# Kernel tuning notes

Measured on AMD Instinct MI355X. Metric: run time of the kernel, lower is better.

## Reference

```python
import jax, jax.numpy as jnp
import numpy as np

LATENT_N = 1024
COMMITMENT_COST = 1.0
TEMP = 0.1


def setup_inputs() -> dict:
    key = jax.random.key(0)
    k0, k1, k2, k3, k4, k5 = jax.random.split(key, 6)
    N, D, H, Fd, K = 65536, 1024, 128, 512, LATENT_N
    input_data = jax.random.normal(k0, (N, D), dtype=jnp.float32)
    W1 = jax.random.normal(k1, (D, H), dtype=jnp.float32) * (1.0 / np.sqrt(D))
    b1 = jnp.zeros((H,), dtype=jnp.float32)
    W2 = jax.random.normal(k2, (H, Fd), dtype=jnp.float32) * (1.0 / np.sqrt(H))
    b2 = jnp.zeros((Fd,), dtype=jnp.float32)
    code_book = jax.random.uniform(k3, (K, Fd), dtype=jnp.float32,
                                   minval=-1.0 / K, maxval=1.0 / K)
    return {"input_data": input_data, "W1": W1, "b1": b1,
            "W2": W2, "b2": b2, "code_book": code_book}


def reference(input_data, W1, b1, W2, b2, code_book):
    # feat MLP: Linear -> ReLU -> Linear
    z = jnp.matmul(jnp.maximum(jnp.matmul(input_data, W1) + b1, 0.0), W2) + b2  # [N, F]
    # squared L2 distances to codebook entries: [N, K]
    distances = (jnp.sum(z * z, axis=1, keepdims=True)
                 + jnp.sum(code_book * code_book, axis=1)
                 - 2.0 * jnp.matmul(z, code_book.T))
    logits = -distances / TEMP
    # categorical sample per row (softmax of logits)
    idx = jax.random.categorical(jax.random.key(42), logits, axis=-1)  # [N] int
    encodings = jax.nn.one_hot(idx, LATENT_N, dtype=z.dtype)  # [N, K]
    quantized = jnp.matmul(encodings, code_book)  # [N, F] == code_book[idx]
    e_latent_loss = jnp.mean((jax.lax.stop_gradient(quantized) - z) ** 2)
    q_latent_loss = jnp.mean((quantized - jax.lax.stop_gradient(z)) ** 2)
    loss = q_latent_loss + COMMITMENT_COST * e_latent_loss
    # straight-through estimator
    quantized_st = z + jax.lax.stop_gradient(quantized - z)
    avg_probs = jnp.mean(encodings, axis=0)  # [K]
    perplexity = jnp.exp(-jnp.sum(avg_probs * jnp.log(avg_probs + 1e-10)))
    return (loss, quantized_st, perplexity, encodings, -distances)
```

## Files before the change

kernel.cpp:

```cpp
#include <hip/hip_runtime.h>
#include <stdint.h>

#define N_ROWS 65536
#define DIM 1024
#define HID 128
#define FD 512
#define KCB 1024
#define HALFCNT 33554432u

#define OFF_Q    1
#define OFF_PERP 33554433
#define OFF_ENC  33554434
#define OFF_ND   100663298

typedef __attribute__((ext_vector_type(8))) short sh8;
typedef __attribute__((ext_vector_type(4))) float f32x4;

__device__ __forceinline__ uint32_t rotl32(uint32_t v, int r) { return (v << r) | (v >> (32 - r)); }

__device__ __forceinline__ void threefry(uint32_t c0, uint32_t c1, uint32_t& o0, uint32_t& o1) {
    const uint32_t ks0 = 0u, ks1 = 42u, ks2 = 0x1BD11BDAu ^ 0u ^ 42u;
    uint32_t x0 = c0 + ks0, x1 = c1 + ks1;
#define TFR(r) x0 += x1; x1 = rotl32(x1, r); x1 ^= x0;
    TFR(13) TFR(15) TFR(26) TFR(6)  x0 += ks1; x1 += ks2 + 1u;
    TFR(17) TFR(29) TFR(16) TFR(24) x0 += ks2; x1 += ks0 + 2u;
    TFR(13) TFR(15) TFR(26) TFR(6)  x0 += ks0; x1 += ks1 + 3u;
    TFR(17) TFR(29) TFR(16) TFR(24) x0 += ks1; x1 += ks2 + 4u;
    TFR(13) TFR(15) TFR(26) TFR(6)  x0 += ks2; x1 += ks0 + 5u;
#undef TFR
    o0 = x0; o1 = x1;
}

__device__ __forceinline__ float gumbel_f32(uint32_t b) {
    uint32_t m = b >> 9;
    float u = m ? (float)m * 1.1920928955078125e-07f : 1.17549435e-38f;
    const float LN2 = 0.6931471805599453f;
    return -LN2 * __log2f(-LN2 * __log2f(u));
}

__device__ __forceinline__ ushort bf16rne(float f) {
    uint32_t u = __float_as_uint(f);
    return (ushort)((u + 0x7FFFu + ((u >> 16) & 1u)) >> 16);
}
__device__ __forceinline__ uint32_t pack2rne(float a, float b) {
    return (uint32_t)bf16rne(a) | ((uint32_t)bf16rne(b) << 16);
}

__device__ __forceinline__ void async_cp16(const void* g, void* l) {
    __builtin_amdgcn_global_load_lds(
        (const __attribute__((address_space(1))) void*)g,
        (__attribute__((address_space(3))) void*)l, 16, 0, 0);
}

__global__ __launch_bounds__(256) void k_prep(const float* __restrict__ cb, const float* __restrict__ W1,
                                              const float* __restrict__ W2,
                                              ushort* __restrict__ cbh, double* __restrict__ cc,
                                              ushort* __restrict__ w1th, ushort* __restrict__ w2th,
                                              int* __restrict__ counts, double* __restrict__ lossb) {
    int gb = blockIdx.x, t = threadIdx.x;
    if (gb < 256) {
        int k = gb * 4 + (t >> 6), l = t & 63;
        const float4* row = (const float4*)(cb + (size_t)k * FD);
        float4 a = row[l * 2], b = row[l * 2 + 1];
        float v[8] = {a.x, a.y, a.z, a.w, b.x, b.y, b.z, b.w};
        double s = 0.0;
        uint32_t hu[4];
        #pragma unroll
        for (int e = 0; e < 4; ++e) {
            hu[e] = pack2rne(v[2 * e], v[2 * e + 1]);
            s = fma((double)v[2 * e], (double)v[2 * e], s);
            s = fma((double)v[2 * e + 1], (double)v[2 * e + 1], s);
        }
        *(uint4*)(cbh + (size_t)k * FD + l * 8) = make_uint4(hu[0], hu[1], hu[2], hu[3]);
        for (int off = 32; off; off >>= 1) s += __shfl_down(s, off, 64);
        if (l == 0) cc[k] = s;
    } else if (gb < 384) {
        int c = gb - 256;
        #pragma unroll
        for (int u = 0; u < 4; ++u) {
            int k = t + u * 256;
            w1th[(size_t)c * DIM + k] = bf16rne(W1[(size_t)k * HID + c]);
        }
    } else if (gb < 640) {
        int c = (gb - 384) * 2 + (t >> 7);
        int tt = t & 127;
        w2th[(size_t)c * HID + tt] = bf16rne(W2[(size_t)tt * FD + c]);
    } else {
        for (int k = t; k < KCB; k += 256) counts[k] = 0;
        lossb[t] = 0.0;
    }
}

__global__ __launch_bounds__(256) void kAB(const float* __restrict__ X, const ushort* __restrict__ w1th,
                                           const float* __restrict__ b1, const ushort* __restrict__ w2th,
                                           const float* __restrict__ b2,
                                           ushort* __restrict__ zbh, float* __restrict__ zz) {
    __shared__ __align__(16) char lds[32768];
    __shared__ float zzp[128][2];
    int t = threadIdx.x;
    int lane = t & 63, w = t >> 6;
    int wr = w >> 1, wc = w & 1;
    int lane15 = lane & 15, lg = lane >> 4;
    int n0 = blockIdx.x * 128;
    f32x4 zero4 = {0.f, 0.f, 0.f, 0.f};
    f32x4 acc[4][4];
    #pragma unroll
    for (int i = 0; i < 4; ++i)
        #pragma unroll
        for (int j = 0; j < 4; ++j) acc[i][j] = zero4;

    int xr = t >> 1;
    int cb0 = (t & 1) * 4;
    int xsw = xr & 7;

    for (int k0 = 0; k0 < DIM; k0 += 64) {
        #pragma unroll
        for (int i = 0; i < 4; ++i) {
            int rr = w * 32 + i * 8;
            int row = rr + (lane >> 3);
            int csrc = (lane & 7) ^ (row & 7);
            size_t goff = (size_t)row * DIM + k0 + csrc * 8;
            async_cp16(w1th + goff, lds + 16384 + rr * 128);
        }
        const float* xp = X + (size_t)(n0 + xr) * DIM + k0 + cb0 * 8;
        #pragma unroll
        for (int c = 0; c < 4; ++c) {
            float4 a = *(const float4*)(xp + c * 8);
            float4 b = *(const float4*)(xp + c * 8 + 4);
            uint4 hv;
            hv.x = pack2rne(a.x, a.y);
            hv.y = pack2rne(a.z, a.w);
            hv.z = pack2rne(b.x, b.y);
            hv.w = pack2rne(b.z, b.w);
            int slot = xr * 128 + (((cb0 + c) ^ xsw) << 4);
            *(uint4*)(lds + slot) = hv;
        }
        __syncthreads();
        #pragma unroll
        for (int kh = 0; kh < 2; ++kh) {
            int ch = kh * 4 + lg;
            sh8 ah[4], bh[4];
            #pragma unroll
            for (int i = 0; i < 4; ++i) {
                int ra = wr * 64 + i * 16 + lane15;
                ah[i] = *(const sh8*)(lds + ra * 128 + ((ch ^ (ra & 7)) << 4));
            }
            #pragma unroll
            for (int j = 0; j < 4; ++j) {
                int rb = wc * 64 + j * 16 + lane15;
                bh[j] = *(const sh8*)(lds + 16384 + rb * 128 + ((ch ^ (rb & 7)) << 4));
            }
            #pragma unroll
            for (int i = 0; i < 4; ++i)
                #pragma unroll
                for (int j = 0; j < 4; ++j)
                    acc[i][j] = __builtin_amdgcn_mfma_f32_16x16x32_bf16(ah[i], bh[j], acc[i][j], 0, 0, 0);
        }
        __syncthreads();
    }
    #pragma unroll
    for (int j = 0; j < 4; ++j) {
        int hcol = wc * 64 + j * 16 + lane15;
        float b1v = b1[hcol];
        int k8 = hcol >> 3, klo = hcol & 7;
        #pragma unroll
        for (int i = 0; i < 4; ++i)
            #pragma unroll
            for (int r = 0; r < 4; ++r) {
                int row = wr * 64 + i * 16 + lg * 4 + r;
                ushort hb = bf16rne(fmaxf(acc[i][j][r] + b1v, 0.f));
                *(ushort*)(lds + row * 256 + ((k8 ^ (row & 7)) << 4) + klo * 2) = hb;
            }
    }
    __syncthreads();
    float zsum[16];
    #pragma unroll
    for (int e = 0; e < 16; ++e) zsum[e] = 0.f;
    for (int c2 = 0; c2 < 4; ++c2) {
        f32x4 acc2[4][4];
        #pragma unroll
        for (int i = 0; i < 4; ++i)
            #pragma unroll
            for (int j = 0; j < 4; ++j) acc2[i][j] = zero4;
        #pragma unroll
        for (int kh = 0; kh < 4; ++kh) {
            int ch = kh * 4 + lg;
            sh8 ah[4], bh[4];
            #pragma unroll
            for (int i = 0; i < 4; ++i) {
                int ra = wr * 64 + i * 16 + lane15;
                ah[i] = *(const sh8*)(lds + ra * 256 + ((ch ^ (ra & 7)) << 4));
            }
            #pragma unroll
            for (int j = 0; j < 4; ++j) {
                int col = c2 * 128 + wc * 64 + j * 16 + lane15;
                bh[j] = *(const sh8*)(w2th + (size_t)col * HID + ch * 8);
            }
            #pragma unroll
            for (int i = 0; i < 4; ++i)
                #pragma unroll
                for (int j = 0; j < 4; ++j)
                    acc2[i][j] = __builtin_amdgcn_mfma_f32_16x16x32_bf16(ah[i], bh[j], acc2[i][j], 0, 0, 0);
        }
        #pragma unroll
        for (int j = 0; j < 4; ++j) {
            int col = c2 * 128 + wc * 64 + j * 16 + lane15;
            float b2v = b2[col];
            #pragma unroll
            for (int i = 0; i < 4; ++i)
                #pragma unroll
                for (int r = 0; r < 4; ++r) {
                    int row = wr * 64 + i * 16 + lg * 4 + r;
                    float v = acc2[i][j][r] + b2v;
                    zbh[(size_t)(n0 + row) * FD + col] = bf16rne(v);
                    zsum[i * 4 + r] = fmaf(v, v, zsum[i * 4 + r]);
                }
        }
    }
    #pragma unroll
    for (int e = 0; e < 16; ++e) {
        float s = zsum[e];
        s += __shfl_xor(s, 1, 64); s += __shfl_xor(s, 2, 64);
        s += __shfl_xor(s, 4, 64); s += __shfl_xor(s, 8, 64);
        if (lane15 == 0) zzp[wr * 64 + (e >> 2) * 16 + lg * 4 + (e & 3)][wc] = s;
    }
    __syncthreads();
    if (t < 128) zz[n0 + t] = zzp[t][0] + zzp[t][1];
}

__global__ __launch_bounds__(256) void k_mfma3s(const ushort* __restrict__ zbh, const ushort* __restrict__ cbh,
                                                const float* __restrict__ zz, const double* __restrict__ cc,
                                                float* __restrict__ nd,
                                                unsigned long long* __restrict__ partials) {
    __shared__ __align__(16) char lds[32768];
    int t = threadIdx.x;
    int lane = t & 63, w = t >> 6;
    int wr = w >> 1, wc = w & 1;
    int bid = blockIdx.x;
    int bm = ((bid >> 6) << 3) | (bid & 7);
    int bkn = (bid >> 3) & 7;
    const ushort* Ahg = zbh + (size_t)bm * 128 * FD;
    const ushort* Bhg = cbh + (size_t)bkn * 128 * FD;

    f32x4 zero4 = {0.f, 0.f, 0.f, 0.f};
    f32x4 acc[4][4];
    #pragma unroll
    for (int i = 0; i < 4; ++i)
        #pragma unroll
        for (int j = 0; j < 4; ++j) acc[i][j] = zero4;

    for (int k0 = 0; k0 < FD; k0 += 64) {
        #pragma unroll
        for (int i = 0; i < 4; ++i) {
            int rr = w * 32 + i * 8;
            int row = rr + (lane >> 3);
            int csrc = (lane & 7) ^ (row & 7);
            size_t goff = (size_t)row * FD + k0 + csrc * 8;
            async_cp16(Ahg + goff, lds + rr * 128);
            async_cp16(Bhg + goff, lds + 16384 + rr * 128);
        }
        __syncthreads();
        #pragma unroll
        for (int kh = 0; kh < 2; ++kh) {
            int ch = kh * 4 + (lane >> 4);
            sh8 ah[4], bh[4];
            #pragma unroll
            for (int i = 0; i < 4; ++i) {
                int ra = wr * 64 + i * 16 + (lane & 15);
                ah[i] = *(const sh8*)(lds + ra * 128 + ((ch ^ (ra & 7)) << 4));
            }
            #pragma unroll
            for (int j = 0; j < 4; ++j) {
                int rb = wc * 64 + j * 16 + (lane & 15);
                bh[j] = *(const sh8*)(lds + 16384 + rb * 128 + ((ch ^ (rb & 7)) << 4));
            }
            #pragma unroll
            for (int i = 0; i < 4; ++i)
                #pragma unroll
                for (int j = 0; j < 4; ++j)
                    acc[i][j] = __builtin_amdgcn_mfma_f32_16x16x32_bf16(ah[i], bh[j], acc[i][j], 0, 0, 0);
        }
        __syncthreads();
    }
    int lane15 = lane & 15, lg = lane >> 4;
    int gcol[4];
    double ccv[4];
    #pragma unroll
    for (int j = 0; j < 4; ++j) {
        gcol[j] = bkn * 128 + wc * 64 + j * 16 + lane15;
        ccv[j] = cc[gcol[j]];
    }
    bool high = bm >= 256;
    uint32_t csub = high ? HALFCNT : 0u;
    #pragma unroll
    for (int i = 0; i < 4; ++i)
        #pragma unroll
        for (int r = 0; r < 4; ++r) {
            int grow = bm * 128 + wr * 64 + i * 16 + lg * 4 + r;
            float zzf = zz[grow];
            double zv = (double)zzf;
            size_t rowoff = (size_t)grow << 10;
            unsigned long long bkey = 0ull;
            #pragma unroll
            for (int j = 0; j < 4; ++j) {
                float ndf = (float)(2.0 * (double)acc[i][j][r] - zv - ccv[j]);
                nd[rowoff + gcol[j]] = ndf;
                uint32_t iflat = (uint32_t)grow * 1024u + (uint32_t)gcol[j];
                uint32_t base = iflat - csub;
                uint32_t r0, r1;
                threefry(base, base + HALFCNT, r0, r1);
                float gv = gumbel_f32(high ? r1 : r0);
                float s = (ndf + zzf) * 10.0f + gv;
                uint32_t ub = __float_as_uint(s);
                ub ^= (uint32_t)(((int32_t)ub >> 31) | 0x80000000);
                unsigned long long key = ((unsigned long long)ub << 32) | (uint32_t)(1023 - gcol[j]);
                if (key > bkey) bkey = key;
            }
            #pragma unroll
            for (int m = 1; m <= 8; m <<= 1) {
                unsigned long long o = __shfl_xor(bkey, m, 64);
                if (o > bkey) bkey = o;
            }
            if (lane15 == 0) partials[(size_t)grow * 16 + bkn * 2 + wc] = bkey;
        }
}

__global__ __launch_bounds__(256) void k_enc2(const unsigned long long* __restrict__ partials,
                                              const float* __restrict__ nd, const float* __restrict__ cb,
                                              float* __restrict__ enc, float* __restrict__ qz,
                                              int* __restrict__ counts, double* __restrict__ lossb) {
    int t = threadIdx.x;
    int n0 = blockIdx.x * 16;
    __shared__ int si[16];
    if (t < 16) {
        int n = n0 + t;
        const unsigned long long* p = partials + (size_t)n * 16;
        unsigned long long best = p[0];
        #pragma unroll
        for (int e = 1; e < 16; ++e) {
            unsigned long long v = p[e];
            if (v > best) best = v;
        }
        int k = 1023 - (int)(best & 0xFFFFFFFFull);
        si[t] = k;
        atomicAdd(&counts[k], 1);
        float ndv = nd[(size_t)n * KCB + k];
        atomicAdd(&lossb[n & 255], -(double)ndv);
    }
    __syncthreads();
    #pragma unroll
    for (int r = 0; r < 16; ++r) {
        int id = si[r];
        int base = t * 4;
        float4 v;
        v.x = (id == base)     ? 1.0f : 0.0f;
        v.y = (id == base + 1) ? 1.0f : 0.0f;
        v.z = (id == base + 2) ? 1.0f : 0.0f;
        v.w = (id == base + 3) ? 1.0f : 0.0f;
        *(float4*)&enc[(size_t)(n0 + r) * KCB + base] = v;
    }
    for (int e = t; e < 16 * 128; e += 256) {
        int r = e >> 7, s = e & 127;
        *(float4*)&qz[(size_t)(n0 + r) * FD + s * 4] =
            *(const float4*)&cb[(size_t)si[r] * FD + s * 4];
    }
}

__global__ void k_scalars(const int* __restrict__ counts, const double* __restrict__ lossb,
                          float* __restrict__ out) {
    int t = threadIdx.x;
    double s = 0.0;
    for (int k = t; k < KCB; k += 256) {
        double p = (double)counts[k] * (1.0 / 65536.0);
        s += p * log(p + 1e-10);
    }
    double lsum = lossb[t];
    for (int off = 32; off; off >>= 1) {
        s += __shfl_down(s, off, 64);
        lsum += __shfl_down(lsum, off, 64);
    }
    __shared__ double red[4], redl[4];
    int lane = t & 63, w = t >> 6;
    if (lane == 0) { red[w] = s; redl[w] = lsum; }
    __syncthreads();
    if (t == 0) {
        double tot = red[0] + red[1] + red[2] + red[3];
        double ltot = redl[0] + redl[1] + redl[2] + redl[3];
        out[OFF_PERP] = (float)exp(-tot);
        out[0] = (float)(ltot * (2.0 / 33554432.0));
    }
}

extern "C" void kernel_launch(void* const* d_in, const int* in_sizes, int n_in,
                              void* d_out, int out_size, void* d_ws, size_t ws_size,
                              hipStream_t stream) {
    const float* X  = (const float*)d_in[0];
    const float* W1 = (const float*)d_in[1];
    const float* b1 = (const float*)d_in[2];
    const float* W2 = (const float*)d_in[3];
    const float* b2 = (const float*)d_in[4];
    const float* cb = (const float*)d_in[5];

    float* out = (float*)d_out;
    float* qz  = out + (size_t)OFF_Q;
    float* enc = out + (size_t)OFF_ENC;
    float* nd  = out + (size_t)OFF_ND;

    float* zz = (float*)d_ws;
    double* cc = (double*)(zz + 65536);
    double* lossb = cc + 1024;
    int* counts = (int*)(lossb + 256);

    bool big_ws = ws_size >= ((size_t)100 << 20);
    char* big = big_ws ? ((char*)d_ws + (1 << 20)) : (char*)(enc + 2);
    unsigned long long* partials = (unsigned long long*)big;
    ushort* ub   = (ushort*)(big + ((size_t)9 << 20));
    ushort* zbh  = ub;
    ushort* cbh  = ub + 33554432;
    ushort* w1th = ub + 34078720;
    ushort* w2th = ub + 34209792;

    k_prep<<<641, 256, 0, stream>>>(cb, W1, W2, cbh, cc, w1th, w2th, counts, lossb);
    kAB<<<512, 256, 0, stream>>>(X, w1th, b1, w2th, b2, zbh, zz);
    k_mfma3s<<<4096, 256, 0, stream>>>(zbh, cbh, zz, cc, nd, partials);
    k_enc2<<<4096, 256, 0, stream>>>(partials, nd, cb, enc, qz, counts, lossb);
    k_scalars<<<1, 256, 0, stream>>>(counts, lossb, out);
}
```

Baseline: 472.1 us.

## Fuse distance GEMM, Gumbel argmax and encoding into one row-block kernel

The distance GEMM, Gumbel-max sampling, partial-argmax merge, one-hot and quantized writes are merged into one kernel. Each block owns 64 rows and loops over all 1024 codebook entries, keeping the z tile in LDS and reading codebook fragments straight from global memory. This drops the partials buffer round trip, the reread of nd for the loss, and one kernel launch. The MLP kernel's row tile is also halved to 64 to launch more blocks. The trade-offs are 64KB of LDS per block, lower occupancy, and codebook operands read from global instead of staged tiles.

```diff
diff --git a/kernel.cpp b/kernel.cpp
--- a/kernel.cpp
+++ b/kernel.cpp
@@ -95,22 +95,22 @@
                                            const float* __restrict__ b1, const ushort* __restrict__ w2th,
                                            const float* __restrict__ b2,
                                            ushort* __restrict__ zbh, float* __restrict__ zz) {
-    __shared__ __align__(16) char lds[32768];
-    __shared__ float zzp[128][2];
+    __shared__ __align__(16) char lds[24576];
+    __shared__ float zzp[64][2];
     int t = threadIdx.x;
     int lane = t & 63, w = t >> 6;
     int wr = w >> 1, wc = w & 1;
     int lane15 = lane & 15, lg = lane >> 4;
-    int n0 = blockIdx.x * 128;
+    int n0 = blockIdx.x * 64;
     f32x4 zero4 = {0.f, 0.f, 0.f, 0.f};
-    f32x4 acc[4][4];
-    #pragma unroll
-    for (int i = 0; i < 4; ++i)
+    f32x4 acc[2][4];
+    #pragma unroll
+    for (int i = 0; i < 2; ++i)
         #pragma unroll
         for (int j = 0; j < 4; ++j) acc[i][j] = zero4;
 
-    int xr = t >> 1;
-    int cb0 = (t & 1) * 4;
+    int xr = t >> 2;
+    int cq = (t & 3) * 2;
     int xsw = xr & 7;
 
     for (int k0 = 0; k0 < DIM; k0 += 64) {
@@ -119,12 +119,11 @@
             int rr = w * 32 + i * 8;
             int row = rr + (lane >> 3);
             int csrc = (lane & 7) ^ (row & 7);
-            size_t goff = (size_t)row * DIM + k0 + csrc * 8;
-            async_cp16(w1th + goff, lds + 16384 + rr * 128);
-        }
-        const float* xp = X + (size_t)(n0 + xr) * DIM + k0 + cb0 * 8;
-        #pragma unroll
-        for (int c = 0; c < 4; ++c) {
+            async_cp16(w1th + (size_t)row * DIM + k0 + csrc * 8, lds + 8192 + rr * 128);
+        }
+        const float* xp = X + (size_t)(n0 + xr) * DIM + k0 + cq * 8;
+        #pragma unroll
+        for (int c = 0; c < 2; ++c) {
             float4 a = *(const float4*)(xp + c * 8);
             float4 b = *(const float4*)(xp + c * 8 + 4);
             uint4 hv;
@@ -132,26 +131,25 @@
             hv.y = pack2rne(a.z, a.w);
             hv.z = pack2rne(b.x, b.y);
             hv.w = pack2rne(b.z, b.w);
-            int slot = xr * 128 + (((cb0 + c) ^ xsw) << 4);
-            *(uint4*)(lds + slot) = hv;
+            *(uint4*)(lds + xr * 128 + (((cq + c) ^ xsw) << 4)) = hv;
         }
         __syncthreads();
         #pragma unroll
         for (int kh = 0; kh < 2; ++kh) {
             int ch = kh * 4 + lg;
-            sh8 ah[4], bh[4];
-            #pragma unroll
-            for (int i = 0; i < 4; ++i) {
-                int ra = wr * 64 + i * 16 + lane15;
+            sh8 ah[2], bh[4];
+            #pragma unroll
+            for (int i = 0; i < 2; ++i) {
+                int ra = wr * 32 + i * 16 + lane15;
                 ah[i] = *(const sh8*)(lds + ra * 128 + ((ch ^ (ra & 7)) << 4));
             }
             #pragma unroll
             for (int j = 0; j < 4; ++j) {
                 int rb = wc * 64 + j * 16 + lane15;
-                bh[j] = *(const sh8*)(lds + 16384 + rb * 128 + ((ch ^ (rb & 7)) << 4));
-            }
-            #pragma unroll
-            for (int i = 0; i < 4; ++i)
+                bh[j] = *(const sh8*)(lds + 8192 + rb * 128 + ((ch ^ (rb & 7)) << 4));
+            }
+            #pragma unroll
+            for (int i = 0; i < 2; ++i)
                 #pragma unroll
                 for (int j = 0; j < 4; ++j)
                     acc[i][j] = __builtin_amdgcn_mfma_f32_16x16x32_bf16(ah[i], bh[j], acc[i][j], 0, 0, 0);
@@ -164,31 +162,31 @@
         float b1v = b1[hcol];
         int k8 = hcol >> 3, klo = hcol & 7;
         #pragma unroll
-        for (int i = 0; i < 4; ++i)
+        for (int i = 0; i < 2; ++i)
             #pragma unroll
             for (int r = 0; r < 4; ++r) {
-                int row = wr * 64 + i * 16 + lg * 4 + r;
+                int row = wr * 32 + i * 16 + lg * 4 + r;
                 ushort hb = bf16rne(fmaxf(acc[i][j][r] + b1v, 0.f));
                 *(ushort*)(lds + row * 256 + ((k8 ^ (row & 7)) << 4) + klo * 2) = hb;
             }
     }
     __syncthreads();
-    float zsum[16];
-    #pragma unroll
-    for (int e = 0; e < 16; ++e) zsum[e] = 0.f;
+    float zsum[8];
+    #pragma unroll
+    for (int e = 0; e < 8; ++e) zsum[e] = 0.f;
     for (int c2 = 0; c2 < 4; ++c2) {
-        f32x4 acc2[4][4];
-        #pragma unroll
-        for (int i = 0; i < 4; ++i)
+        f32x4 acc2[2][4];
+        #pragma unroll
+        for (int i = 0; i < 2; ++i)
             #pragma unroll
             for (int j = 0; j < 4; ++j) acc2[i][j] = zero4;
         #pragma unroll
         for (int kh = 0; kh < 4; ++kh) {
             int ch = kh * 4 + lg;
-            sh8 ah[4], bh[4];
-            #pragma unroll
-            for (int i = 0; i < 4; ++i) {
-                int ra = wr * 64 + i * 16 + lane15;
+            sh8 ah[2], bh[4];
+            #pragma unroll
+            for (int i = 0; i < 2; ++i) {
+                int ra = wr * 32 + i * 16 + lane15;
                 ah[i] = *(const sh8*)(lds + ra * 256 + ((ch ^ (ra & 7)) << 4));
             }
             #pragma unroll
@@ -197,7 +195,7 @@
                 bh[j] = *(const sh8*)(w2th + (size_t)col * HID + ch * 8);
             }
             #pragma unroll
-            for (int i = 0; i < 4; ++i)
+            for (int i = 0; i < 2; ++i)
                 #pragma unroll
                 for (int j = 0; j < 4; ++j)
                     acc2[i][j] = __builtin_amdgcn_mfma_f32_16x16x32_bf16(ah[i], bh[j], acc2[i][j], 0, 0, 0);
@@ -207,10 +205,10 @@
             int col = c2 * 128 + wc * 64 + j * 16 + lane15;
             float b2v = b2[col];
             #pragma unroll
-            for (int i = 0; i < 4; ++i)
+            for (int i = 0; i < 2; ++i)
                 #pragma unroll
                 for (int r = 0; r < 4; ++r) {
-                    int row = wr * 64 + i * 16 + lg * 4 + r;
+                    int row = wr * 32 + i * 16 + lg * 4 + r;
                     float v = acc2[i][j][r] + b2v;
                     zbh[(size_t)(n0 + row) * FD + col] = bf16rne(v);
                     zsum[i * 4 + r] = fmaf(v, v, zsum[i * 4 + r]);
@@ -218,135 +216,167 @@
         }
     }
     #pragma unroll
-    for (int e = 0; e < 16; ++e) {
+    for (int e = 0; e < 8; ++e) {
         float s = zsum[e];
         s += __shfl_xor(s, 1, 64); s += __shfl_xor(s, 2, 64);
         s += __shfl_xor(s, 4, 64); s += __shfl_xor(s, 8, 64);
-        if (lane15 == 0) zzp[wr * 64 + (e >> 2) * 16 + lg * 4 + (e & 3)][wc] = s;
-    }
-    __syncthreads();
-    if (t < 128) zz[n0 + t] = zzp[t][0] + zzp[t][1];
-}
-
-__global__ __launch_bounds__(256) void k_mfma3s(const ushort* __restrict__ zbh, const ushort* __restrict__ cbh,
-                                                const float* __restrict__ zz, const double* __restrict__ cc,
-                                                float* __restrict__ nd,
-                                                unsigned long long* __restrict__ partials) {
-    __shared__ __align__(16) char lds[32768];
+        if (lane15 == 0) zzp[wr * 32 + (e >> 2) * 16 + lg * 4 + (e & 3)][wc] = s;
+    }
+    __syncthreads();
+    if (t < 64) zz[n0 + t] = zzp[t][0] + zzp[t][1];
+}
+
+__global__ __launch_bounds__(256) void kDSE(const ushort* __restrict__ zbh, const ushort* __restrict__ cbh,
+                                            const float* __restrict__ zz, const double* __restrict__ cc,
+                                            const float* __restrict__ cbf,
+                                            float* __restrict__ nd, float* __restrict__ enc,
+                                            float* __restrict__ qz, int* __restrict__ idx,
+                                            int* __restrict__ counts, double* __restrict__ lossb,
+                                            int inline_enc) {
+    __shared__ __align__(16) char lds[65536];
     int t = threadIdx.x;
     int lane = t & 63, w = t >> 6;
-    int wr = w >> 1, wc = w & 1;
-    int bid = blockIdx.x;
-    int bm = ((bid >> 6) << 3) | (bid & 7);
-    int bkn = (bid >> 3) & 7;
-    const ushort* Ahg = zbh + (size_t)bm * 128 * FD;
-    const ushort* Bhg = cbh + (size_t)bkn * 128 * FD;
-
+    int lane15 = lane & 15, lg = lane >> 4;
+    int bm = blockIdx.x;
+    int n0 = bm * 64;
+    #pragma unroll
+    for (int i = 0; i < 16; ++i) {
+        int row = w * 16 + i;
+        int csrc = lane ^ (row & 7);
+        async_cp16(zbh + (size_t)(n0 + row) * FD + csrc * 8, lds + row * 1024);
+    }
+    __syncthreads();
+    float zzr[16];
+    #pragma unroll
+    for (int e = 0; e < 16; ++e)
+        zzr[e] = zz[n0 + (e >> 2) * 16 + lg * 4 + (e & 3)];
+    unsigned long long bkey[16];
+    float bnd[16];
+    #pragma unroll
+    for (int e = 0; e < 16; ++e) { bkey[e] = 0ull; bnd[e] = 0.f; }
+    bool high = n0 >= 32768;
+    uint32_t csub = high ? HALFCNT : 0u;
     f32x4 zero4 = {0.f, 0.f, 0.f, 0.f};
-    f32x4 acc[4][4];
-    #pragma unroll
-    for (int i = 0; i < 4; ++i)
-        #pragma unroll
-        for (int j = 0; j < 4; ++j) acc[i][j] = zero4;
-
-    for (int k0 = 0; k0 < FD; k0 += 64) {
-        #pragma unroll
-        for (int i = 0; i < 4; ++i) {
-            int rr = w * 32 + i * 8;
-            int row = rr + (lane >> 3);
-            int csrc = (lane & 7) ^ (row & 7);
-            size_t goff = (size_t)row * FD + k0 + csrc * 8;
-            async_cp16(Ahg + goff, lds + rr * 128);
-            async_cp16(Bhg + goff, lds + 16384 + rr * 128);
-        }
-        __syncthreads();
-        #pragma unroll
-        for (int kh = 0; kh < 2; ++kh) {
-            int ch = kh * 4 + (lane >> 4);
-            sh8 ah[4], bh[4];
+
+    for (int bkn = 0; bkn < 8; ++bkn) {
+        f32x4 acc[4][2];
+        #pragma unroll
+        for (int i = 0; i < 4; ++i) { acc[i][0] = zero4; acc[i][1] = zero4; }
+        #pragma unroll
+        for (int ks = 0; ks < 16; ++ks) {
+            int ch = ks * 4 + lg;
+            sh8 ah[4], bh[2];
             #pragma unroll
             for (int i = 0; i < 4; ++i) {
-                int ra = wr * 64 + i * 16 + (lane & 15);
-                ah[i] = *(const sh8*)(lds + ra * 128 + ((ch ^ (ra & 7)) << 4));
-            }
-            #pragma unroll
-            for (int j = 0; j < 4; ++j) {
-                int rb = wc * 64 + j * 16 + (lane & 15);
-                bh[j] = *(const sh8*)(lds + 16384 + rb * 128 + ((ch ^ (rb & 7)) << 4));
-            }
-            #pragma unroll
-            for (int i = 0; i < 4; ++i)
+                int ra = i * 16 + lane15;
+                ah[i] = *(const sh8*)(lds + ra * 1024 + ((ch ^ (ra & 7)) << 4));
+            }
+            #pragma unroll
+            for (int j = 0; j < 2; ++j) {
+                int col = bkn * 128 + w * 32 + j * 16 + lane15;
+                bh[j] = *(const sh8*)(cbh + (size_t)col * FD + ch * 8);
+            }
+            #pragma unroll
+            for (int i = 0; i < 4; ++i) {
+                acc[i][0] = __builtin_amdgcn_mfma_f32_16x16x32_bf16(ah[i], bh[0], acc[i][0], 0, 0, 0);
+                acc[i][1] = __builtin_amdgcn_mfma_f32_16x16x32_bf16(ah[i], bh[1], acc[i][1], 0, 0, 0);
+            }
+        }
+        int gcol0 = bkn * 128 + w * 32 + lane15;
+        double ccv0 = cc[gcol0], ccv1 = cc[gcol0 + 16];
+        #pragma unroll
+        for (int i = 0; i < 4; ++i)
+            #pragma unroll
+            for (int r = 0; r < 4; ++r) {
+                int e = i * 4 + r;
+                int grow = n0 + i * 16 + lg * 4 + r;
+                float zzf = zzr[e];
+                double zv = (double)zzf;
+                size_t rowoff = (size_t)grow << 10;
                 #pragma unroll
-                for (int j = 0; j < 4; ++j)
-                    acc[i][j] = __builtin_amdgcn_mfma_f32_16x16x32_bf16(ah[i], bh[j], acc[i][j], 0, 0, 0);
-        }
-        __syncthreads();
-    }
-    int lane15 = lane & 15, lg = lane >> 4;
-    int gcol[4];
-    double ccv[4];
-    #pragma unroll
-    for (int j = 0; j < 4; ++j) {
-        gcol[j] = bkn * 128 + wc * 64 + j * 16 + lane15;
-        ccv[j] = cc[gcol[j]];
-    }
-    bool high = bm >= 256;
-    uint32_t csub = high ? HALFCNT : 0u;
-    #pragma unroll
-    for (int i = 0; i < 4; ++i)
-        #pragma unroll
-        for (int r = 0; r < 4; ++r) {
-            int grow = bm * 128 + wr * 64 + i * 16 + lg * 4 + r;
-            float zzf = zz[grow];
-            double zv = (double)zzf;
-            size_t rowoff = (size_t)grow << 10;
-            unsigned long long bkey = 0ull;
-            #pragma unroll
-            for (int j = 0; j < 4; ++j) {
-                float ndf = (float)(2.0 * (double)acc[i][j][r] - zv - ccv[j]);
-                nd[rowoff + gcol[j]] = ndf;
-                uint32_t iflat = (uint32_t)grow * 1024u + (uint32_t)gcol[j];
-                uint32_t base = iflat - csub;
-                uint32_t r0, r1;
-                threefry(base, base + HALFCNT, r0, r1);
-                float gv = gumbel_f32(high ? r1 : r0);
-                float s = (ndf + zzf) * 10.0f + gv;
-                uint32_t ub = __float_as_uint(s);
-                ub ^= (uint32_t)(((int32_t)ub >> 31) | 0x80000000);
-                unsigned long long key = ((unsigned long long)ub << 32) | (uint32_t)(1023 - gcol[j]);
-                if (key > bkey) bkey = key;
-            }
-            #pragma unroll
-            for (int m = 1; m <= 8; m <<= 1) {
-                unsigned long long o = __shfl_xor(bkey, m, 64);
-                if (o > bkey) bkey = o;
-            }
-            if (lane15 == 0) partials[(size_t)grow * 16 + bkn * 2 + wc] = bkey;
-        }
-}
-
-__global__ __launch_bounds__(256) void k_enc2(const unsigned long long* __restrict__ partials,
-                                              const float* __restrict__ nd, const float* __restrict__ cb,
-                                              float* __restrict__ enc, float* __restrict__ qz,
-                                              int* __restrict__ counts, double* __restrict__ lossb) {
+                for (int j = 0; j < 2; ++j) {
+                    int gcol = gcol0 + j * 16;
+                    float ndf = (float)(2.0 * (double)acc[i][j][r] - zv - (j ? ccv1 : ccv0));
+                    nd[rowoff + gcol] = ndf;
+                    uint32_t base = (uint32_t)grow * 1024u + (uint32_t)gcol - csub;
+                    uint32_t r0, r1;
+                    threefry(base, base + HALFCNT, r0, r1);
+                    float gv = gumbel_f32(high ? r1 : r0);
+                    float s = (ndf + zzf) * 10.0f + gv;
+                    uint32_t ub = __float_as_uint(s);
+                    ub ^= (uint32_t)(((int32_t)ub >> 31) | 0x80000000);
+                    unsigned long long key = ((unsigned long long)ub << 32) | (uint32_t)(1023 - gcol);
+                    if (key > bkey[e]) { bkey[e] = key; bnd[e] = ndf; }
+                }
+            }
+    }
+    #pragma unroll
+    for (int e = 0; e < 16; ++e) {
+        unsigned long long k = bkey[e];
+        float nv = bnd[e];
+        #pragma unroll
+        for (int m = 1; m <= 8; m <<= 1) {
+            unsigned long long ok = __shfl_xor(k, m, 64);
+            float on = __shfl_xor(nv, m, 64);
+            if (ok > k) { k = ok; nv = on; }
+        }
+        bkey[e] = k; bnd[e] = nv;
+    }
+    __syncthreads();
+    unsigned long long (*rk)[4] = (unsigned long long (*)[4])lds;
+    float (*rn)[4] = (float (*)[4])(lds + 2048);
+    int* si = (int*)(lds + 3072);
+    if (lane15 == 0) {
+        #pragma unroll
+        for (int e = 0; e < 16; ++e) {
+            int row = (e >> 2) * 16 + lg * 4 + (e & 3);
+            rk[row][w] = bkey[e];
+            rn[row][w] = bnd[e];
+        }
+    }
+    __syncthreads();
+    if (t < 64) {
+        unsigned long long best = rk[t][0];
+        float nv = rn[t][0];
+        #pragma unroll
+        for (int e = 1; e < 4; ++e) {
+            if (rk[t][e] > best) { best = rk[t][e]; nv = rn[t][e]; }
+        }
+        int k = 1023 - (int)(best & 0xFFFFFFFFull);
+        si[t] = k;
+        idx[n0 + t] = k;
+        atomicAdd(&counts[k], 1);
+        double dl = -(double)nv;
+        for (int off = 32; off; off >>= 1) dl += __shfl_down(dl, off, 64);
+        if (t == 0) atomicAdd(&lossb[bm & 255], dl);
+    }
+    __syncthreads();
+    if (inline_enc) {
+        #pragma unroll 4
+        for (int r = 0; r < 64; ++r) {
+            int id = si[r];
+            int base = t * 4;
+            float4 v;
+            v.x = (id == base)     ? 1.0f : 0.0f;
+            v.y = (id == base + 1) ? 1.0f : 0.0f;
+            v.z = (id == base + 2) ? 1.0f : 0.0f;
+            v.w = (id == base + 3) ? 1.0f : 0.0f;
+            *(float4*)&enc[(size_t)(n0 + r) * KCB + base] = v;
+        }
+        for (int e = t; e < 64 * 128; e += 256) {
+            int r = e >> 7, s2 = e & 127;
+            *(float4*)&qz[(size_t)(n0 + r) * FD + s2 * 4] =
+                *(const float4*)&cbf[(size_t)si[r] * FD + s2 * 4];
+        }
+    }
+}
+
+__global__ __launch_bounds__(256) void k_encF(const int* __restrict__ idx, const float* __restrict__ cb,
+                                              float* __restrict__ enc, float* __restrict__ qz) {
     int t = threadIdx.x;
     int n0 = blockIdx.x * 16;
     __shared__ int si[16];
-    if (t < 16) {
-        int n = n0 + t;
-        const unsigned long long* p = partials + (size_t)n * 16;
-        unsigned long long best = p[0];
-        #pragma unroll
-        for (int e = 1; e < 16; ++e) {
-            unsigned long long v = p[e];
-            if (v > best) best = v;
-        }
-        int k = 1023 - (int)(best & 0xFFFFFFFFull);
-        si[t] = k;
-        atomicAdd(&counts[k], 1);
-        float ndv = nd[(size_t)n * KCB + k];
-        atomicAdd(&lossb[n & 255], -(double)ndv);
-    }
+    if (t < 16) si[t] = idx[n0 + t];
     __syncthreads();
     #pragma unroll
     for (int r = 0; r < 16; ++r) {
@@ -410,19 +440,20 @@
     double* cc = (double*)(zz + 65536);
     double* lossb = cc + 1024;
     int* counts = (int*)(lossb + 256);
+    int* idx = counts + 1024;
 
     bool big_ws = ws_size >= ((size_t)100 << 20);
     char* big = big_ws ? ((char*)d_ws + (1 << 20)) : (char*)(enc + 2);
-    unsigned long long* partials = (unsigned long long*)big;
-    ushort* ub   = (ushort*)(big + ((size_t)9 << 20));
+    ushort* ub   = (ushort*)big;
     ushort* zbh  = ub;
     ushort* cbh  = ub + 33554432;
     ushort* w1th = ub + 34078720;
     ushort* w2th = ub + 34209792;
 
     k_prep<<<641, 256, 0, stream>>>(cb, W1, W2, cbh, cc, w1th, w2th, counts, lossb);
-    kAB<<<512, 256, 0, stream>>>(X, w1th, b1, w2th, b2, zbh, zz);
-    k_mfma3s<<<4096, 256, 0, stream>>>(zbh, cbh, zz, cc, nd, partials);
-    k_enc2<<<4096, 256, 0, stream>>>(partials, nd, cb, enc, qz, counts, lossb);
+    kAB<<<1024, 256, 0, stream>>>(X, w1th, b1, w2th, b2, zbh, zz);
+    kDSE<<<1024, 256, 0, stream>>>(zbh, cbh, zz, cc, cb, nd, enc, qz, idx, counts, lossb,
+                                   big_ws ? 1 : 0);
+    if (!big_ws) k_encF<<<4096, 256, 0, stream>>>(idx, cb, enc, qz);
     k_scalars<<<1, 256, 0, stream>>>(counts, lossb, out);
 }
```

New measurement: 664.5 us. 1.41x slower.
